# Optimization experiments

Measured on AMD Instinct MI355X. Metric: run time of the kernel, lower is better.

## Reference

```python
import jax, jax.numpy as jnp
import numpy as np

GAMMA = 0.5
POLY_COEF = 0.1
POLY_DEGREE = 3


def setup_inputs() -> dict:
    key = jax.random.key(0)
    kx, ky = jax.random.split(key)
    x = jax.random.normal(kx, (8192, 256), dtype=jnp.float32)
    y = jax.random.normal(ky, (8192, 256), dtype=jnp.float32)
    return {"x": x, "y": y}


def reference(x, y):
    # K(x, y) = exp(-gamma * ||x - y||^2) + poly_coef * (x.y^T + 1)^degree
    xy = x @ y.T                                   # (N, M) GEMM
    x2 = jnp.sum(x * x, axis=-1, keepdims=True)    # (N, 1)
    y2 = jnp.sum(y * y, axis=-1)[None, :]          # (1, M)
    sqdist = jnp.maximum(x2 + y2 - 2.0 * xy, 0.0)
    rbf = jnp.exp(-GAMMA * sqdist)
    poly = POLY_COEF * (xy + 1.0) ** POLY_DEGREE
    return rbf + poly
```

## Files before the change

### kernel.cpp

```cpp
#include <hip/hip_runtime.h>
#include <hip/hip_bf16.h>
#include <cstdint>
#include <cstddef>


#define NROWS 8192
#define DK    256
#define BM    128
#define BN    128
#define BK    32

typedef __bf16 bf16_8 __attribute__((ext_vector_type(8)));
typedef float  f32x4  __attribute__((ext_vector_type(4)));

__device__ __forceinline__ unsigned short f2bf(float f) {
    unsigned int u = __builtin_bit_cast(unsigned int, f);
    u = (u + 0x7FFFu + ((u >> 16) & 1u)) >> 16;
    return (unsigned short)u;
}

__global__ __launch_bounds__(64) void prep_kernel(
    const float* __restrict__ x, const float* __restrict__ y,
    unsigned short* __restrict__ xb, unsigned short* __restrict__ yb,
    float* __restrict__ x2, float* __restrict__ y2)
{
    const int row  = blockIdx.x;
    const int lane = threadIdx.x;
    const size_t base = (size_t)row * DK + lane * 4;

    const float4 vx = *(const float4*)(x + base);
    const float4 vy = *(const float4*)(y + base);

    ushort4 hx = make_ushort4(f2bf(vx.x), f2bf(vx.y), f2bf(vx.z), f2bf(vx.w));
    ushort4 hy = make_ushort4(f2bf(vy.x), f2bf(vy.y), f2bf(vy.z), f2bf(vy.w));
    *(ushort4*)(xb + base) = hx;
    *(ushort4*)(yb + base) = hy;

    float sx = vx.x * vx.x + vx.y * vx.y + vx.z * vx.z + vx.w * vx.w;
    float sy = vy.x * vy.x + vy.y * vy.y + vy.z * vy.z + vy.w * vy.w;
    #pragma unroll
    for (int off = 32; off > 0; off >>= 1) {
        sx += __shfl_down(sx, off);
        sy += __shfl_down(sy, off);
    }
    if (lane == 0) {
        x2[row] = sx;
        y2[row] = sy;
    }
}

__global__ __launch_bounds__(256) void gemm_ep_kernel(
    const unsigned short* __restrict__ xb, const unsigned short* __restrict__ yb,
    const float* __restrict__ x2, const float* __restrict__ y2,
    float* __restrict__ out)
{
    __shared__ __align__(16) unsigned short As[BM * BK];
    __shared__ __align__(16) unsigned short Bs[BN * BK];

    const int tid  = threadIdx.x;
    const int wave = tid >> 6;
    const int lane = tid & 63;
    const int bm   = blockIdx.x;
    const int bn   = blockIdx.y;

    const int wm = (wave & 1) * 64;
    const int wn = (wave >> 1) * 64;

    const int c0   = wave * 2;
    const int c1   = c0 + 1;
    const int lrow = lane >> 2;
    const int lcol = (lane & 3) * 8;

    const unsigned short* gA0 = xb + (size_t)(bm * BM + c0 * 16 + lrow) * DK + lcol;
    const unsigned short* gA1 = xb + (size_t)(bm * BM + c1 * 16 + lrow) * DK + lcol;
    const unsigned short* gB0 = yb + (size_t)(bn * BN + c0 * 16 + lrow) * DK + lcol;
    const unsigned short* gB1 = yb + (size_t)(bn * BN + c1 * 16 + lrow) * DK + lcol;
    unsigned short* lA0 = &As[c0 * 512];
    unsigned short* lA1 = &As[c1 * 512];
    unsigned short* lB0 = &Bs[c0 * 512];
    unsigned short* lB1 = &Bs[c1 * 512];

    f32x4 acc[4][4];
    #pragma unroll
    for (int i = 0; i < 4; ++i)
        #pragma unroll
        for (int j = 0; j < 4; ++j)
            acc[i][j] = (f32x4){0.f, 0.f, 0.f, 0.f};

    const int quad = lane >> 4;
    const int l15  = lane & 15;

    for (int kt = 0; kt < DK; kt += BK) {
        __builtin_amdgcn_global_load_lds(
            (const __attribute__((address_space(1))) void*)(gA0 + kt),
            (__attribute__((address_space(3))) void*)lA0, 16, 0, 0);
        __builtin_amdgcn_global_load_lds(
            (const __attribute__((address_space(1))) void*)(gA1 + kt),
            (__attribute__((address_space(3))) void*)lA1, 16, 0, 0);
        __builtin_amdgcn_global_load_lds(
            (const __attribute__((address_space(1))) void*)(gB0 + kt),
            (__attribute__((address_space(3))) void*)lB0, 16, 0, 0);
        __builtin_amdgcn_global_load_lds(
            (const __attribute__((address_space(1))) void*)(gB1 + kt),
            (__attribute__((address_space(3))) void*)lB1, 16, 0, 0);
        __syncthreads();

        bf16_8 afr[4], bfr[4];
        #pragma unroll
        for (int i = 0; i < 4; ++i)
            afr[i] = *(const bf16_8*)&As[(wm + i * 16 + l15) * BK + quad * 8];
        #pragma unroll
        for (int j = 0; j < 4; ++j)
            bfr[j] = *(const bf16_8*)&Bs[(wn + j * 16 + l15) * BK + quad * 8];

        #pragma unroll
        for (int i = 0; i < 4; ++i)
            #pragma unroll
            for (int j = 0; j < 4; ++j)
                acc[i][j] = __builtin_amdgcn_mfma_f32_16x16x32_bf16(
                    afr[i], bfr[j], acc[i][j], 0, 0, 0);
        __syncthreads();
    }

    const int mBase = bm * BM + wm + quad * 4;
    const int nBase = bn * BN + wn + l15;

    float y2v[4];
    #pragma unroll
    for (int j = 0; j < 4; ++j) y2v[j] = y2[nBase + j * 16];

    #pragma unroll
    for (int i = 0; i < 4; ++i) {
        #pragma unroll
        for (int r = 0; r < 4; ++r) {
            const int m = mBase + i * 16 + r;
            const float xv = x2[m];
            float* orow = out + (size_t)m * NROWS + nBase;
            #pragma unroll
            for (int j = 0; j < 4; ++j) {
                const float xy = acc[i][j][r];
                float s = xv + y2v[j] - 2.0f * xy;
                s = fmaxf(s, 0.0f);
                const float e = __expf(-0.5f * s);
                const float p = xy + 1.0f;
                orow[j * 16] = fmaf(0.1f, p * p * p, e);
            }
        }
    }
}

extern "C" void kernel_launch(void* const* d_in, const int* in_sizes, int n_in,
                              void* d_out, int out_size, void* d_ws, size_t ws_size,
                              hipStream_t stream) {
    const float* x = (const float*)d_in[0];
    const float* y = (const float*)d_in[1];
    float* out = (float*)d_out;

    char* ws = (char*)d_ws;
    unsigned short* xb = (unsigned short*)ws;
    unsigned short* yb = (unsigned short*)(ws + (size_t)NROWS * DK * 2);
    float* x2 = (float*)(ws + (size_t)2 * NROWS * DK * 2);
    float* y2 = x2 + NROWS;

    prep_kernel<<<NROWS, 64, 0, stream>>>(x, y, xb, yb, x2, y2);

    dim3 grid(NROWS / BM, NROWS / BN);
    gemm_ep_kernel<<<grid, 256, 0, stream>>>(xb, yb, x2, y2, out);
}
```

Before: 295.8 us.

## Double GEMM K-tile to 64 with XOR-swizzled LDS layout

Raises the K tile from 32 to 64, which halves the number of load/barrier iterations, and fully unrolls the K loop. Each tile stage now runs two MFMA sub-steps. Global-to-LDS loads use an XOR swizzle on the 16-byte slot index, and the fragment reads apply the same XOR, to avoid LDS bank conflicts from the wider row stride. LDS use doubles to 32 KB per block, which may lower occupancy, and there is still no double buffering.

```diff
diff --git a/kernel.cpp b/kernel.cpp
--- a/kernel.cpp
+++ b/kernel.cpp
@@ -8,7 +8,7 @@
 #define DK    256
 #define BM    128
 #define BN    128
-#define BK    32
+#define BK    64
 
 typedef __bf16 bf16_8 __attribute__((ext_vector_type(8)));
 typedef float  f32x4  __attribute__((ext_vector_type(4)));
@@ -66,19 +66,22 @@
     const int wm = (wave & 1) * 64;
     const int wn = (wave >> 1) * 64;
 
-    const int c0   = wave * 2;
-    const int c1   = c0 + 1;
-    const int lrow = lane >> 2;
-    const int lcol = (lane & 3) * 8;
+    const int subrow = lane >> 3;
+    const int sslot  = (lane & 7) ^ subrow;
+    const size_t laneoff = (size_t)subrow * DK + sslot * 8;
 
-    const unsigned short* gA0 = xb + (size_t)(bm * BM + c0 * 16 + lrow) * DK + lcol;
-    const unsigned short* gA1 = xb + (size_t)(bm * BM + c1 * 16 + lrow) * DK + lcol;
-    const unsigned short* gB0 = yb + (size_t)(bn * BN + c0 * 16 + lrow) * DK + lcol;
-    const unsigned short* gB1 = yb + (size_t)(bn * BN + c1 * 16 + lrow) * DK + lcol;
-    unsigned short* lA0 = &As[c0 * 512];
-    unsigned short* lA1 = &As[c1 * 512];
-    unsigned short* lB0 = &Bs[c0 * 512];
-    unsigned short* lB1 = &Bs[c1 * 512];
+    const unsigned short* gA[4];
+    const unsigned short* gB[4];
+    unsigned short* lA[4];
+    unsigned short* lB[4];
+    #pragma unroll
+    for (int m = 0; m < 4; ++m) {
+        const int c = wave * 4 + m;
+        gA[m] = xb + (size_t)(bm * BM + c * 8) * DK + laneoff;
+        gB[m] = yb + (size_t)(bn * BN + c * 8) * DK + laneoff;
+        lA[m] = &As[c * 512];
+        lB[m] = &Bs[c * 512];
+    }
 
     f32x4 acc[4][4];
     #pragma unroll
@@ -89,36 +92,42 @@
 
     const int quad = lane >> 4;
     const int l15  = lane & 15;
+    const int l7   = l15 & 7;
 
+    const int rbaseA = (wm + l15) * BK;
+    const int rbaseB = (wn + l15) * BK;
+
+    #pragma unroll
     for (int kt = 0; kt < DK; kt += BK) {
-        __builtin_amdgcn_global_load_lds(
-            (const __attribute__((address_space(1))) void*)(gA0 + kt),
-            (__attribute__((address_space(3))) void*)lA0, 16, 0, 0);
-        __builtin_amdgcn_global_load_lds(
-            (const __attribute__((address_space(1))) void*)(gA1 + kt),
-            (__attribute__((address_space(3))) void*)lA1, 16, 0, 0);
-        __builtin_amdgcn_global_load_lds(
-            (const __attribute__((address_space(1))) void*)(gB0 + kt),
-            (__attribute__((address_space(3))) void*)lB0, 16, 0, 0);
-        __builtin_amdgcn_global_load_lds(
-            (const __attribute__((address_space(1))) void*)(gB1 + kt),
-            (__attribute__((address_space(3))) void*)lB1, 16, 0, 0);
+        #pragma unroll
+        for (int m = 0; m < 4; ++m) {
+            __builtin_amdgcn_global_load_lds(
+                (const __attribute__((address_space(1))) void*)(gA[m] + kt),
+                (__attribute__((address_space(3))) void*)lA[m], 16, 0, 0);
+            __builtin_amdgcn_global_load_lds(
+                (const __attribute__((address_space(1))) void*)(gB[m] + kt),
+                (__attribute__((address_space(3))) void*)lB[m], 16, 0, 0);
+        }
         __syncthreads();
 
-        bf16_8 afr[4], bfr[4];
         #pragma unroll
-        for (int i = 0; i < 4; ++i)
-            afr[i] = *(const bf16_8*)&As[(wm + i * 16 + l15) * BK + quad * 8];
-        #pragma unroll
-        for (int j = 0; j < 4; ++j)
-            bfr[j] = *(const bf16_8*)&Bs[(wn + j * 16 + l15) * BK + quad * 8];
-
-        #pragma unroll
-        for (int i = 0; i < 4; ++i)
+        for (int kk = 0; kk < 2; ++kk) {
+            const int slot = ((kk << 2) | quad) ^ l7;
+            bf16_8 afr[4], bfr[4];
+            #pragma unroll
+            for (int i = 0; i < 4; ++i)
+                afr[i] = *(const bf16_8*)&As[rbaseA + i * 16 * BK + slot * 8];
             #pragma unroll
             for (int j = 0; j < 4; ++j)
-                acc[i][j] = __builtin_amdgcn_mfma_f32_16x16x32_bf16(
-                    afr[i], bfr[j], acc[i][j], 0, 0, 0);
+                bfr[j] = *(const bf16_8*)&Bs[rbaseB + j * 16 * BK + slot * 8];
+
+            #pragma unroll
+            for (int i = 0; i < 4; ++i)
+                #pragma unroll
+                for (int j = 0; j < 4; ++j)
+                    acc[i][j] = __builtin_amdgcn_mfma_f32_16x16x32_bf16(
+                        afr[i], bfr[j], acc[i][j], 0, 0, 0);
+        }
         __syncthreads();
     }
 
```

Result: no change. 290.3 us (-1.9%).
